# Optimization experiments

Hardware: AMD Instinct MI355X
Metric: run time of the kernel (lower is better)

Reference implementation:

```python
import jax, jax.numpy as jnp
import numpy as np

B, T, C, H = 4, 4096, 1024, 64  # batch, seq, n_embd, head_size

def setup_inputs() -> dict:
    key = jax.random.key(0)
    kx, kq, kk, kv = jax.random.split(key, 4)
    x = jax.random.normal(kx, (B, T, C), dtype=jnp.float32)
    s = 1.0 / np.sqrt(C)
    Wq = jax.random.normal(kq, (C, H), dtype=jnp.float32) * s
    Wk = jax.random.normal(kk, (C, H), dtype=jnp.float32) * s
    Wv = jax.random.normal(kv, (C, H), dtype=jnp.float32) * s
    return {"x": x, "Wq": Wq, "Wk": Wk, "Wv": Wv}

def reference(x, Wq, Wk, Wv):
    B_, T_, C_ = x.shape
    q = x @ Wq  # [B,T,H]
    k = x @ Wk
    v = x @ Wv
    # NOTE: original scales by C**-0.5 (n_embd), not head_size**-0.5
    scale = jnp.asarray(C_, x.dtype) ** -0.5
    wei = jnp.einsum('bth,bsh->bts', q, k) * scale  # [B,T,T]
    causal = jnp.tril(jnp.ones((T_, T_), dtype=bool))
    wei = jnp.where(causal, wei, -jnp.inf)
    wei = jax.nn.softmax(wei, axis=-1)
    out = jnp.einsum('bts,bsh->bth', wei, v)  # [B,T,H]
    return out
```

## Files before the change

### kernel.cpp

```cpp
#include <hip/hip_runtime.h>
#include <hip/hip_bf16.h>
#include <math.h>

#define BB 4
#define TT 4096
#define CC 1024
#define HH 64

typedef __attribute__((ext_vector_type(8))) short short8;
typedef __attribute__((ext_vector_type(8))) unsigned short ushort8;
typedef __attribute__((ext_vector_type(4))) float f32x4;
typedef __attribute__((ext_vector_type(2))) unsigned int uint2v;

__device__ inline unsigned short f2bf(float f) {
    unsigned int u = __builtin_bit_cast(unsigned int, f);
    unsigned int r = u + 0x7fffu + ((u >> 16) & 1u);
    return (unsigned short)(r >> 16);
}

__device__ inline int soff_strip(int qs) {
    if (qs < 128) return (qs - 64) * 2;
    if (qs < 192) return 128 + (qs - 128) * 3;
    return 320 + (qs - 192) * 4;
}

__global__ __launch_bounds__(256) void wtrans_kernel(
    const float* __restrict__ Wq,
    const float* __restrict__ Wk,
    const float* __restrict__ Wv,
    unsigned short* __restrict__ Wf)
{
    const int t = blockIdx.x * 256 + threadIdx.x;
    const int lane = t & 63;
    const int ntl  = (t >> 6) % 12;
    const int kt   = t / 768;
    const int quad = lane >> 4, n = lane & 15;
    const int m    = ntl >> 2;
    const int col  = (ntl & 3) * 16 + n;
    const float* src = (m == 0) ? Wq : (m == 1) ? Wk : Wv;
    ushort8 u;
#pragma unroll
    for (int j = 0; j < 8; ++j)
        u[j] = f2bf(src[(kt * 32 + quad * 8 + j) * 64 + col]);
    *(ushort8*)(Wf + (size_t)t * 8) = u;
}

__global__ __launch_bounds__(256) void qkv_gemm(
    const float* __restrict__ x,
    const unsigned short* __restrict__ Wf,
    unsigned short* __restrict__ Qb,
    unsigned short* __restrict__ Kb,
    unsigned short* __restrict__ Vb)
{
    __shared__ f32x4 red[4][12][64];

    const int tid  = threadIdx.x;
    const int lane = tid & 63;
    const int wave = tid >> 6;
    const int n    = lane & 15;
    const int quad = lane >> 4;
    const int row0 = blockIdx.x * 16;

    const float* xp = x + (size_t)(row0 + n) * CC + wave * 256 + quad * 8;

    f32x4 acc[12];
#pragma unroll
    for (int i = 0; i < 12; ++i) acc[i] = (f32x4){0.f, 0.f, 0.f, 0.f};

#pragma unroll
    for (int kt = 0; kt < 8; ++kt) {
        const float4 f0 = *(const float4*)(xp + kt * 32);
        const float4 f1 = *(const float4*)(xp + kt * 32 + 4);
        short8 a;
        a[0] = (short)f2bf(f0.x); a[1] = (short)f2bf(f0.y);
        a[2] = (short)f2bf(f0.z); a[3] = (short)f2bf(f0.w);
        a[4] = (short)f2bf(f1.x); a[5] = (short)f2bf(f1.y);
        a[6] = (short)f2bf(f1.z); a[7] = (short)f2bf(f1.w);

        const unsigned short* wp = Wf + ((size_t)((wave * 8 + kt) * 12) * 64 + lane) * 8;
#pragma unroll
        for (int ntl = 0; ntl < 12; ++ntl) {
            const short8 bw = *(const short8*)(wp + (size_t)ntl * 64 * 8);
            acc[ntl] = __builtin_amdgcn_mfma_f32_16x16x32_bf16(a, bw, acc[ntl], 0, 0, 0);
        }
    }

#pragma unroll
    for (int ntl = 0; ntl < 12; ++ntl) red[wave][ntl][lane] = acc[ntl];
    __syncthreads();

#pragma unroll
    for (int i = 0; i < 3; ++i) {
        const int ntl = wave * 3 + i;
        f32x4 s = red[0][ntl][lane];
        s += red[1][ntl][lane];
        s += red[2][ntl][lane];
        s += red[3][ntl][lane];
        const int m    = ntl >> 2;
        const int colb = (ntl & 3) * 16;
        unsigned short* dst = (m == 0) ? Qb : (m == 1) ? Kb : Vb;
        const float sc = (m == 0) ? 0.03125f : 1.0f;
#pragma unroll
        for (int r = 0; r < 4; ++r) {
            const int row = row0 + quad * 4 + r;
            dst[(size_t)row * HH + colb + n] = f2bf(s[r] * sc);
        }
    }
}

__global__ __launch_bounds__(256) void kv_repack(
    const unsigned short* __restrict__ Kb,
    const unsigned short* __restrict__ Vb,
    unsigned short* __restrict__ Kf,
    unsigned short* __restrict__ Vf)
{
    const int t = blockIdx.x * 256 + threadIdx.x;
    const int mat  = t >> 17;
    const int r    = t & 131071;
    const int lane = r & 63;
    const int kk   = (r >> 6) & 1;
    const int tile = (r >> 7) & 3;
    const int st   = (r >> 9) & 63;
    const int b    = r >> 15;
    const int n = lane & 15, quad = lane >> 4;

    if (mat == 0) {
        const unsigned short* src =
            Kb + ((size_t)b * TT + st * 64 + tile * 16 + n) * HH + kk * 32 + quad * 8;
        *(ushort8*)(Kf + (size_t)r * 8) = *(const ushort8*)src;
    } else {
        const int s0 = st * 64 + kk * 32 + quad * 8;
        const int h  = tile * 16 + n;
        ushort8 u;
#pragma unroll
        for (int j = 0; j < 8; ++j)
            u[j] = Vb[((size_t)b * TT + s0 + j) * HH + h];
        *(ushort8*)(Vf + (size_t)r * 8) = u;
    }
}

__global__ __launch_bounds__(256) void attn_kernel(
    const unsigned short* __restrict__ Qb,
    const unsigned short* __restrict__ Kf,
    const unsigned short* __restrict__ Vf,
    float* __restrict__ out,
    float* __restrict__ scr)
{
    __shared__ unsigned short Ps[4][16][72];

    const int tid  = threadIdx.x;
    const int lane = tid & 63;
    const int wave = tid >> 6;
    const int n    = lane & 15;
    const int quad = lane >> 4;

    const int wid = blockIdx.x * 4 + wave;
    const int b   = wid >> 10;
    const int rem = wid & 1023;
    const int qs  = rem >> 2;
    const int ci  = rem & 3;
    const int stmax = qs >> 2;
    const int nc  = (stmax + 16) >> 4;
    if (ci >= nc) return;
    const int st0   = ci << 4;
    const int stEnd = min(stmax, st0 + 15);

    const int qrow = qs * 16 + n;

    const unsigned short* qp = Qb + ((size_t)b * TT + qrow) * HH;
    const short8 bQ0 = *(const short8*)(qp + quad * 8);
    const short8 bQ1 = *(const short8*)(qp + 32 + quad * 8);

    const unsigned short* KfB = Kf + (size_t)b * 262144;
    const unsigned short* VfB = Vf + (size_t)b * 262144;

    f32x4 O[4];
#pragma unroll
    for (int ht = 0; ht < 4; ++ht) O[ht] = (f32x4){0.f, 0.f, 0.f, 0.f};
    float l = 0.f;

    for (int st = st0; st <= stEnd; ++st) {
        f32x4 S[4];
#pragma unroll
        for (int mt = 0; mt < 4; ++mt) {
            const unsigned short* kp = KfB + (size_t)((st * 4 + mt) * 2) * 512 + lane * 8;
            const short8 a0 = *(const short8*)(kp);
            const short8 a1 = *(const short8*)(kp + 512);
            f32x4 acc = (f32x4){0.f, 0.f, 0.f, 0.f};
            acc = __builtin_amdgcn_mfma_f32_16x16x32_bf16(a0, bQ0, acc, 0, 0, 0);
            acc = __builtin_amdgcn_mfma_f32_16x16x32_bf16(a1, bQ1, acc, 0, 0, 0);
            S[mt] = acc;
        }

        if (st == stmax) {
#pragma unroll
            for (int mt = 0; mt < 4; ++mt) {
                const int sg = st * 64 + mt * 16 + quad * 4;
#pragma unroll
                for (int r = 0; r < 4; ++r)
                    if (sg + r > qrow) S[mt][r] = -INFINITY;
            }
        }

#pragma unroll
        for (int mt = 0; mt < 4; ++mt)
#pragma unroll
            for (int r = 0; r < 4; ++r) {
                const float p = __expf(fminf(S[mt][r], 30.f));
                S[mt][r] = p;
                l += p;
            }

#pragma unroll
        for (int mt = 0; mt < 4; ++mt) {
            uint2v w;
            w[0] = (unsigned int)f2bf(S[mt][0]) | ((unsigned int)f2bf(S[mt][1]) << 16);
            w[1] = (unsigned int)f2bf(S[mt][2]) | ((unsigned int)f2bf(S[mt][3]) << 16);
            *(uint2v*)&Ps[wave][n][mt * 16 + quad * 4] = w;
        }
        asm volatile("s_waitcnt lgkmcnt(0)" ::: "memory");
        const short8 bP0 = *(const short8*)&Ps[wave][n][quad * 8];
        const short8 bP1 = *(const short8*)&Ps[wave][n][32 + quad * 8];

#pragma unroll
        for (int ht = 0; ht < 4; ++ht) {
            const unsigned short* vp = VfB + (size_t)((st * 4 + ht) * 2) * 512 + lane * 8;
            const short8 a0 = *(const short8*)(vp);
            const short8 a1 = *(const short8*)(vp + 512);
            O[ht] = __builtin_amdgcn_mfma_f32_16x16x32_bf16(a0, bP0, O[ht], 0, 0, 0);
            O[ht] = __builtin_amdgcn_mfma_f32_16x16x32_bf16(a1, bP1, O[ht], 0, 0, 0);
        }
    }

    l += __shfl_xor(l, 16);
    l += __shfl_xor(l, 32);

    if (nc == 1) {
        const float inv = 1.0f / l;
        float* op = out + ((size_t)b * TT + qrow) * HH;
#pragma unroll
        for (int ht = 0; ht < 4; ++ht) {
            float4 o4;
            o4.x = O[ht][0] * inv;
            o4.y = O[ht][1] * inv;
            o4.z = O[ht][2] * inv;
            o4.w = O[ht][3] * inv;
            *(float4*)(op + ht * 16 + quad * 4) = o4;
        }
    } else {
        float* sb = scr + (size_t)(b * 576 + soff_strip(qs) + ci) * 1040;
        float* rp = sb + n * 64;
#pragma unroll
        for (int ht = 0; ht < 4; ++ht)
            *(f32x4*)(rp + ht * 16 + quad * 4) = O[ht];
        if (quad == 0) sb[1024 + n] = l;
    }
}

__global__ __launch_bounds__(64) void combine_kernel(
    const float* __restrict__ scr,
    float* __restrict__ out)
{
    const int b  = blockIdx.x / 192;
    const int qs = 64 + blockIdx.x % 192;
    const int nc = ((qs >> 2) + 16) >> 4;
    const int base = b * 576 + soff_strip(qs);

    const int t    = threadIdx.x;
    const int row  = t >> 2;
    const int col0 = (t & 3) * 16;

    f32x4 s0 = (f32x4){0.f,0.f,0.f,0.f}, s1 = s0, s2 = s0, s3 = s0;
    float lsum = 0.f;
    for (int ci = 0; ci < nc; ++ci) {
        const float* sb = scr + (size_t)(base + ci) * 1040;
        lsum += sb[1024 + row];
        const float* p = sb + row * 64 + col0;
        s0 += *(const f32x4*)(p);
        s1 += *(const f32x4*)(p + 4);
        s2 += *(const f32x4*)(p + 8);
        s3 += *(const f32x4*)(p + 12);
    }
    const float inv = 1.0f / lsum;
    float* op = out + ((size_t)b * TT + qs * 16 + row) * HH + col0;
    *(f32x4*)(op)      = s0 * inv;
    *(f32x4*)(op + 4)  = s1 * inv;
    *(f32x4*)(op + 8)  = s2 * inv;
    *(f32x4*)(op + 12) = s3 * inv;
}

extern "C" void kernel_launch(void* const* d_in, const int* in_sizes, int n_in,
                              void* d_out, int out_size, void* d_ws, size_t ws_size,
                              hipStream_t stream)
{
    const float* x  = (const float*)d_in[0];
    const float* Wq = (const float*)d_in[1];
    const float* Wk = (const float*)d_in[2];
    const float* Wv = (const float*)d_in[3];

    unsigned short* Qb = (unsigned short*)d_ws;
    float*          scr = (float*)(Qb + (size_t)BB * TT * HH);
    unsigned short* Kb  = (unsigned short*)scr;
    unsigned short* Vb  = Kb + (size_t)BB * TT * HH;
    unsigned short* Wf  = (unsigned short*)((char*)scr + (size_t)BB * 576 * 1040 * 4);
    unsigned short* Kf  = Wf + (size_t)192 * 1024;
    unsigned short* Vf  = Kf + (size_t)BB * 262144;
    float* out = (float*)d_out;

    wtrans_kernel<<<96, 256, 0, stream>>>(Wq, Wk, Wv, Wf);
    qkv_gemm<<<BB * TT / 16, 256, 0, stream>>>(x, Wf, Qb, Kb, Vb);
    kv_repack<<<1024, 256, 0, stream>>>(Kb, Vb, Kf, Vf);
    attn_kernel<<<1024, 256, 0, stream>>>(Qb, Kf, Vf, out, scr);
    combine_kernel<<<768, 64, 0, stream>>>(scr, out);
}
```

Baseline: 160.1 us.

## Retile QKV GEMM, read K directly, and group attention waves by key range

The QKV projection now has each block handle 32 rows with a 2x2 wave split over rows and K-halves. This halves the cross-wave reduction and reuses each weight fragment across two row groups. The K repack is removed, and attention loads K straight from its row-major bf16 layout, since that already matches the MFMA operand layout. Attention blocks now hold four consecutive query strips that share one key chunk range, so waves in a block reuse the same K/V tiles in cache and exit early together. The risks are a non-unrolled K loop in the GEMM and fewer GEMM blocks.

```diff
diff --git a/kernel.cpp b/kernel.cpp
--- a/kernel.cpp
+++ b/kernel.cpp
@@ -59,16 +59,17 @@
     const int wave = tid >> 6;
     const int n    = lane & 15;
     const int quad = lane >> 4;
-    const int row0 = blockIdx.x * 16;
-
-    const float* xp = x + (size_t)(row0 + n) * CC + wave * 256 + quad * 8;
+    const int rg   = wave & 1;
+    const int kh   = wave >> 1;
+    const int row0 = blockIdx.x * 32;
+
+    const float* xp = x + (size_t)(row0 + rg * 16 + n) * CC + kh * 512 + quad * 8;
 
     f32x4 acc[12];
 #pragma unroll
     for (int i = 0; i < 12; ++i) acc[i] = (f32x4){0.f, 0.f, 0.f, 0.f};
 
-#pragma unroll
-    for (int kt = 0; kt < 8; ++kt) {
+    for (int kt = 0; kt < 16; ++kt) {
         const float4 f0 = *(const float4*)(xp + kt * 32);
         const float4 f1 = *(const float4*)(xp + kt * 32 + 4);
         short8 a;
@@ -77,7 +78,8 @@
         a[4] = (short)f2bf(f1.x); a[5] = (short)f2bf(f1.y);
         a[6] = (short)f2bf(f1.z); a[7] = (short)f2bf(f1.w);
 
-        const unsigned short* wp = Wf + ((size_t)((wave * 8 + kt) * 12) * 64 + lane) * 8;
+        const int ktg = kh * 16 + kt;
+        const unsigned short* wp = Wf + ((size_t)(ktg * 12) * 64 + lane) * 8;
 #pragma unroll
         for (int ntl = 0; ntl < 12; ++ntl) {
             const short8 bw = *(const short8*)(wp + (size_t)ntl * 64 * 8);
@@ -89,34 +91,30 @@
     for (int ntl = 0; ntl < 12; ++ntl) red[wave][ntl][lane] = acc[ntl];
     __syncthreads();
 
-#pragma unroll
-    for (int i = 0; i < 3; ++i) {
-        const int ntl = wave * 3 + i;
-        f32x4 s = red[0][ntl][lane];
-        s += red[1][ntl][lane];
-        s += red[2][ntl][lane];
-        s += red[3][ntl][lane];
+    const int erg = wave & 1;
+    const int nb  = (wave >> 1) * 6;
+#pragma unroll
+    for (int i = 0; i < 6; ++i) {
+        const int ntl = nb + i;
+        f32x4 s = red[erg][ntl][lane];
+        s += red[erg + 2][ntl][lane];
         const int m    = ntl >> 2;
         const int colb = (ntl & 3) * 16;
         unsigned short* dst = (m == 0) ? Qb : (m == 1) ? Kb : Vb;
         const float sc = (m == 0) ? 0.03125f : 1.0f;
 #pragma unroll
         for (int r = 0; r < 4; ++r) {
-            const int row = row0 + quad * 4 + r;
+            const int row = row0 + erg * 16 + quad * 4 + r;
             dst[(size_t)row * HH + colb + n] = f2bf(s[r] * sc);
         }
     }
 }
 
-__global__ __launch_bounds__(256) void kv_repack(
-    const unsigned short* __restrict__ Kb,
+__global__ __launch_bounds__(256) void v_repack(
     const unsigned short* __restrict__ Vb,
-    unsigned short* __restrict__ Kf,
     unsigned short* __restrict__ Vf)
 {
-    const int t = blockIdx.x * 256 + threadIdx.x;
-    const int mat  = t >> 17;
-    const int r    = t & 131071;
+    const int r = blockIdx.x * 256 + threadIdx.x;
     const int lane = r & 63;
     const int kk   = (r >> 6) & 1;
     const int tile = (r >> 7) & 3;
@@ -124,28 +122,28 @@
     const int b    = r >> 15;
     const int n = lane & 15, quad = lane >> 4;
 
-    if (mat == 0) {
-        const unsigned short* src =
-            Kb + ((size_t)b * TT + st * 64 + tile * 16 + n) * HH + kk * 32 + quad * 8;
-        *(ushort8*)(Kf + (size_t)r * 8) = *(const ushort8*)src;
-    } else {
-        const int s0 = st * 64 + kk * 32 + quad * 8;
-        const int h  = tile * 16 + n;
-        ushort8 u;
-#pragma unroll
-        for (int j = 0; j < 8; ++j)
-            u[j] = Vb[((size_t)b * TT + s0 + j) * HH + h];
-        *(ushort8*)(Vf + (size_t)r * 8) = u;
-    }
+    const int s0 = st * 64 + kk * 32 + quad * 8;
+    const int h  = tile * 16 + n;
+    ushort8 u;
+#pragma unroll
+    for (int j = 0; j < 8; ++j)
+        u[j] = Vb[((size_t)b * TT + s0 + j) * HH + h];
+    *(ushort8*)(Vf + (size_t)r * 8) = u;
 }
 
 __global__ __launch_bounds__(256) void attn_kernel(
     const unsigned short* __restrict__ Qb,
-    const unsigned short* __restrict__ Kf,
+    const unsigned short* __restrict__ Kb,
     const unsigned short* __restrict__ Vf,
     float* __restrict__ out,
     float* __restrict__ scr)
 {
+    const int b  = blockIdx.x >> 8;
+    const int g  = (blockIdx.x >> 2) & 63;
+    const int ci = blockIdx.x & 3;
+    const int nc = (g + 16) >> 4;
+    if (ci >= nc) return;
+
     __shared__ unsigned short Ps[4][16][72];
 
     const int tid  = threadIdx.x;
@@ -154,24 +152,17 @@
     const int n    = lane & 15;
     const int quad = lane >> 4;
 
-    const int wid = blockIdx.x * 4 + wave;
-    const int b   = wid >> 10;
-    const int rem = wid & 1023;
-    const int qs  = rem >> 2;
-    const int ci  = rem & 3;
-    const int stmax = qs >> 2;
-    const int nc  = (stmax + 16) >> 4;
-    if (ci >= nc) return;
+    const int qs    = g * 4 + wave;
+    const int stmax = g;
     const int st0   = ci << 4;
     const int stEnd = min(stmax, st0 + 15);
-
-    const int qrow = qs * 16 + n;
+    const int qrow  = qs * 16 + n;
 
     const unsigned short* qp = Qb + ((size_t)b * TT + qrow) * HH;
     const short8 bQ0 = *(const short8*)(qp + quad * 8);
     const short8 bQ1 = *(const short8*)(qp + 32 + quad * 8);
 
-    const unsigned short* KfB = Kf + (size_t)b * 262144;
+    const unsigned short* KbB = Kb + (size_t)b * TT * HH;
     const unsigned short* VfB = Vf + (size_t)b * 262144;
 
     f32x4 O[4];
@@ -183,9 +174,9 @@
         f32x4 S[4];
 #pragma unroll
         for (int mt = 0; mt < 4; ++mt) {
-            const unsigned short* kp = KfB + (size_t)((st * 4 + mt) * 2) * 512 + lane * 8;
+            const unsigned short* kp = KbB + (size_t)(st * 64 + mt * 16 + n) * HH + quad * 8;
             const short8 a0 = *(const short8*)(kp);
-            const short8 a1 = *(const short8*)(kp + 512);
+            const short8 a1 = *(const short8*)(kp + 32);
             f32x4 acc = (f32x4){0.f, 0.f, 0.f, 0.f};
             acc = __builtin_amdgcn_mfma_f32_16x16x32_bf16(a0, bQ0, acc, 0, 0, 0);
             acc = __builtin_amdgcn_mfma_f32_16x16x32_bf16(a1, bQ1, acc, 0, 0, 0);
@@ -299,17 +290,16 @@
     const float* Wv = (const float*)d_in[3];
 
     unsigned short* Qb = (unsigned short*)d_ws;
-    float*          scr = (float*)(Qb + (size_t)BB * TT * HH);
-    unsigned short* Kb  = (unsigned short*)scr;
-    unsigned short* Vb  = Kb + (size_t)BB * TT * HH;
-    unsigned short* Wf  = (unsigned short*)((char*)scr + (size_t)BB * 576 * 1040 * 4);
-    unsigned short* Kf  = Wf + (size_t)192 * 1024;
-    unsigned short* Vf  = Kf + (size_t)BB * 262144;
+    unsigned short* Kb = Qb + (size_t)BB * TT * HH;
+    unsigned short* Vb = Kb + (size_t)BB * TT * HH;
+    unsigned short* Wf = Vb + (size_t)BB * TT * HH;
+    unsigned short* Vf = Wf + (size_t)192 * 1024;
+    float*          scr = (float*)(Vf + (size_t)BB * 262144);
     float* out = (float*)d_out;
 
     wtrans_kernel<<<96, 256, 0, stream>>>(Wq, Wk, Wv, Wf);
-    qkv_gemm<<<BB * TT / 16, 256, 0, stream>>>(x, Wf, Qb, Kb, Vb);
-    kv_repack<<<1024, 256, 0, stream>>>(Kb, Vb, Kf, Vf);
-    attn_kernel<<<1024, 256, 0, stream>>>(Qb, Kf, Vf, out, scr);
+    qkv_gemm<<<BB * TT / 32, 256, 0, stream>>>(x, Wf, Qb, Kb, Vb);
+    v_repack<<<512, 256, 0, stream>>>(Vb, Vf);
+    attn_kernel<<<BB * 64 * 4, 256, 0, stream>>>(Qb, Kb, Vf, out, scr);
     combine_kernel<<<768, 64, 0, stream>>>(scr, out);
 }
```

Measured after the change: 225.7 us. 41.0% more time.

## Compact attention work mapping to skip idle waves and tree-reduce QKV partials

Applied to the files above, without the earlier changes.

The attention launch now maps waves only to (query strip, chunk) pairs that carry real work, so the grid shrinks from 1024 to 640 blocks and no waves exit early. The QKV GEMM cross-wave reduction becomes a two-step tree through a half-sized shared buffer, with wave 0 doing all stores. The workspace layout is rearranged so the scratch buffer no longer overlaps K/V staging. The aim is to cut wasted wave launches and LDS footprint. In exchange the final QKV stores are serialized on one wave and an extra barrier is added.

```diff
diff --git a/kernel.cpp b/kernel.cpp
--- a/kernel.cpp
+++ b/kernel.cpp
@@ -52,7 +52,7 @@
     unsigned short* __restrict__ Kb,
     unsigned short* __restrict__ Vb)
 {
-    __shared__ f32x4 red[4][12][64];
+    __shared__ f32x4 red[2][12][64];
 
     const int tid  = threadIdx.x;
     const int lane = tid & 63;
@@ -85,25 +85,34 @@
         }
     }
 
-#pragma unroll
-    for (int ntl = 0; ntl < 12; ++ntl) red[wave][ntl][lane] = acc[ntl];
+    if (wave >= 2) {
+#pragma unroll
+        for (int ntl = 0; ntl < 12; ++ntl) red[wave - 2][ntl][lane] = acc[ntl];
+    }
     __syncthreads();
-
-#pragma unroll
-    for (int i = 0; i < 3; ++i) {
-        const int ntl = wave * 3 + i;
-        f32x4 s = red[0][ntl][lane];
-        s += red[1][ntl][lane];
-        s += red[2][ntl][lane];
-        s += red[3][ntl][lane];
-        const int m    = ntl >> 2;
-        const int colb = (ntl & 3) * 16;
-        unsigned short* dst = (m == 0) ? Qb : (m == 1) ? Kb : Vb;
-        const float sc = (m == 0) ? 0.03125f : 1.0f;
-#pragma unroll
-        for (int r = 0; r < 4; ++r) {
-            const int row = row0 + quad * 4 + r;
-            dst[(size_t)row * HH + colb + n] = f2bf(s[r] * sc);
+    if (wave < 2) {
+#pragma unroll
+        for (int ntl = 0; ntl < 12; ++ntl) acc[ntl] += red[wave][ntl][lane];
+    }
+    __syncthreads();
+    if (wave == 1) {
+#pragma unroll
+        for (int ntl = 0; ntl < 12; ++ntl) red[0][ntl][lane] = acc[ntl];
+    }
+    __syncthreads();
+    if (wave == 0) {
+#pragma unroll
+        for (int ntl = 0; ntl < 12; ++ntl) {
+            f32x4 s = acc[ntl] + red[0][ntl][lane];
+            const int m    = ntl >> 2;
+            const int colb = (ntl & 3) * 16;
+            unsigned short* dst = (m == 0) ? Qb : (m == 1) ? Kb : Vb;
+            const float sc = (m == 0) ? 0.03125f : 1.0f;
+#pragma unroll
+            for (int r = 0; r < 4; ++r) {
+                const int row = row0 + quad * 4 + r;
+                dst[(size_t)row * HH + colb + n] = f2bf(s[r] * sc);
+            }
         }
     }
 }
@@ -155,17 +164,21 @@
     const int quad = lane >> 4;
 
     const int wid = blockIdx.x * 4 + wave;
-    const int b   = wid >> 10;
-    const int rem = wid & 1023;
-    const int qs  = rem >> 2;
-    const int ci  = rem & 3;
+    const int b   = wid / 640;
+    const int u   = wid - b * 640;
+
+    int qs, ci;
+    if (u < 64)        { qs = u;                  ci = 0; }
+    else if (u < 192)  { const int v = u - 64;  qs = 64  + (v >> 1); ci = v & 1; }
+    else if (u < 384)  { const int v = u - 192; const int d = v / 3;
+                         qs = 128 + d;            ci = v - 3 * d; }
+    else               { const int v = u - 384; qs = 192 + (v >> 2); ci = v & 3; }
+
     const int stmax = qs >> 2;
-    const int nc  = (stmax + 16) >> 4;
-    if (ci >= nc) return;
     const int st0   = ci << 4;
     const int stEnd = min(stmax, st0 + 15);
-
-    const int qrow = qs * 16 + n;
+    const int nc    = (stmax + 16) >> 4;
+    const int qrow  = qs * 16 + n;
 
     const unsigned short* qp = Qb + ((size_t)b * TT + qrow) * HH;
     const short8 bQ0 = *(const short8*)(qp + quad * 8);
@@ -299,17 +312,17 @@
     const float* Wv = (const float*)d_in[3];
 
     unsigned short* Qb = (unsigned short*)d_ws;
-    float*          scr = (float*)(Qb + (size_t)BB * TT * HH);
-    unsigned short* Kb  = (unsigned short*)scr;
-    unsigned short* Vb  = Kb + (size_t)BB * TT * HH;
-    unsigned short* Wf  = (unsigned short*)((char*)scr + (size_t)BB * 576 * 1040 * 4);
-    unsigned short* Kf  = Wf + (size_t)192 * 1024;
-    unsigned short* Vf  = Kf + (size_t)BB * 262144;
+    unsigned short* Kb = Qb + (size_t)BB * TT * HH;
+    unsigned short* Vb = Kb + (size_t)BB * TT * HH;
+    unsigned short* Wf = Vb + (size_t)BB * TT * HH;
+    unsigned short* Kf = Wf + (size_t)192 * 1024;
+    unsigned short* Vf = Kf + (size_t)BB * 262144;
+    float*          scr = (float*)(Vf + (size_t)BB * 262144);
     float* out = (float*)d_out;
 
     wtrans_kernel<<<96, 256, 0, stream>>>(Wq, Wk, Wv, Wf);
     qkv_gemm<<<BB * TT / 16, 256, 0, stream>>>(x, Wf, Qb, Kb, Vb);
     kv_repack<<<1024, 256, 0, stream>>>(Kb, Vb, Kf, Vf);
-    attn_kernel<<<1024, 256, 0, stream>>>(Qb, Kf, Vf, out, scr);
+    attn_kernel<<<640, 256, 0, stream>>>(Qb, Kf, Vf, out, scr);
     combine_kernel<<<768, 64, 0, stream>>>(scr, out);
 }
```

Result: no change. 160.0 us (-0.1%).
